# Kernel optimization log

Hardware: AMD Instinct MI355X
Metric: run time of the kernel (lower is better)

The kernel has to match this reference:

```python
import jax, jax.numpy as jnp
import numpy as np

FREQ_DIM = 32
TIME_DIM = 32
HEADS = 8
TWO_PI = 6.283185307179586


def get_embeddings(B, H, W, freq_dim, time_dim, dtype):
    # freq embeddings over the height (frequency) axis
    nf = freq_dim // 2
    ln_x = jnp.log2(jnp.arange(0, H * nf, dtype=jnp.float32))
    ln_x = ln_x.at[0].set(-2.0)
    ln_x = ln_x.reshape(H, nf).T  # [nf, H]
    ln_x = ln_x * jnp.arange(1, nf + 1, dtype=jnp.float32)[:, None]
    # view_as_real(exp(1j*theta)) -> (cos, sin), interleaved per order along channel dim
    freq = jnp.stack([jnp.cos(ln_x), jnp.sin(ln_x)], axis=1).reshape(freq_dim, H)  # [freq_dim, H]
    freq = jnp.broadcast_to(freq[None, :, :, None], (B, freq_dim, H, W))

    # time embeddings over the width (time) axis
    nt = time_dim // 2
    k = jnp.arange(0, nt, dtype=jnp.float32) + 0.5  # [nt]
    x = jnp.arange(0, nt * W, dtype=jnp.float32).reshape(W, nt).T  # [nt, W]
    theta = k[:, None] * x / (W * nt) * TWO_PI  # [nt, W]
    time = jnp.stack([jnp.cos(theta), jnp.sin(theta)], axis=1).reshape(time_dim, W)  # [time_dim, W]
    time = jnp.broadcast_to(time[None, :, None, :], (B, time_dim, H, W))

    return jnp.concatenate([freq, time], axis=1).astype(dtype)  # [B, freq_dim+time_dim, H, W]


def setup_inputs() -> dict:
    key = jax.random.key(0)
    ks = jax.random.split(key, 6)
    B, C, H, W = 2, 512, 64, 32
    qkC = C + FREQ_DIM + TIME_DIM  # 576
    inner = HEADS * 64  # 512
    return {
        "hidden_states": jax.random.normal(ks[0], (B, C, H, W), dtype=jnp.float32),
        "Wq": jax.random.normal(ks[1], (qkC, inner), dtype=jnp.float32) * 0.02,
        "Wk": jax.random.normal(ks[2], (qkC, inner), dtype=jnp.float32) * 0.02,
        "Wv": jax.random.normal(ks[3], (C, inner), dtype=jnp.float32) * 0.02,
        "Wout": jax.random.normal(ks[4], (inner, C), dtype=jnp.float32) * 0.02,
        "bout": jnp.zeros((C,), dtype=jnp.float32),
    }


def reference(hidden_states, Wq, Wk, Wv, Wout, bout):
    B, C, H, W = hidden_states.shape
    emb = get_embeddings(B, H, W, FREQ_DIM, TIME_DIM, hidden_states.dtype)
    qk_hs = jnp.concatenate([hidden_states, emb], axis=1)  # [B, qkC, H, W]

    S = H * W
    qk_hs = qk_hs.reshape(B, -1, S).transpose(0, 2, 1)  # [B, S, qkC]
    v_hs = hidden_states.reshape(B, C, S).transpose(0, 2, 1)  # [B, S, C]

    q = qk_hs @ Wq  # [B, S, inner]
    k = qk_hs @ Wk
    v = v_hs @ Wv

    hd_qk = q.shape[-1] // HEADS
    hd_v = v.shape[-1] // HEADS
    q = q.reshape(B, S, HEADS, hd_qk).transpose(0, 2, 1, 3)  # [B, h, S, d]
    k = k.reshape(B, S, HEADS, hd_qk).transpose(0, 2, 1, 3)
    v = v.reshape(B, S, HEADS, hd_v).transpose(0, 2, 1, 3)

    scale = 1.0 / jnp.sqrt(jnp.asarray(hd_qk, dtype=q.dtype))
    scores = jnp.einsum('bhqd,bhkd->bhqk', q, k) * scale
    attn = jax.nn.softmax(scores, axis=-1)
    o = jnp.einsum('bhqk,bhkd->bhqd', attn, v)  # [B, h, S, d_v]

    o = o.transpose(0, 2, 1, 3).reshape(B, S, HEADS * hd_v)
    o = o @ Wout + bout  # [B, S, C]
    o = o.transpose(0, 2, 1).reshape(B, C, H, W)

    return o + hidden_states  # residual_connection=True, rescale_output_factor=1.0
```

## Files before the change

kernel.cpp:

```cpp
#include <hip/hip_runtime.h>
#include <math.h>

#define B_    2
#define C_    512
#define H_    64
#define W_    32
#define S_    2048
#define QKC_  576
#define INNER_ 512
#define NH_   8
#define HD_   64
#define TWO_PI_ 6.283185307179586f

typedef __attribute__((ext_vector_type(8))) short bfrag;
typedef __attribute__((ext_vector_type(4))) float ffrag;
typedef __attribute__((ext_vector_type(16))) float f16v;

typedef __attribute__((address_space(1))) const unsigned int as1_u32;
typedef __attribute__((address_space(3))) unsigned int as3_u32;

__device__ __forceinline__ ushort f2bf(float f) {
    unsigned u = __builtin_bit_cast(unsigned, f);
    unsigned r = (u + 0x7FFFu + ((u >> 16) & 1u)) >> 16;
    return (ushort)r;
}

__device__ __forceinline__ f16v zero16() {
    f16v z;
    #pragma unroll
    for (int i = 0; i < 16; i++) z[i] = 0.f;
    return z;
}

#define GLD(gp_, lp_) __builtin_amdgcn_global_load_lds((as1_u32*)(gp_), (as3_u32*)(lp_), 16, 0, 0)
#define EXPA(dst_, x_) asm("v_exp_f32 %0, %1" : "=v"(dst_) : "v"(x_))
#define SC_LOG2E 0.18033688011f

__global__ void k_pre(const float* __restrict__ hid,
                      const float* __restrict__ Wq, const float* __restrict__ Wk,
                      const float* __restrict__ Wv, const float* __restrict__ Wo,
                      ushort* __restrict__ X,
                      ushort* __restrict__ Wqt, ushort* __restrict__ Wkt,
                      ushort* __restrict__ Wvt, ushort* __restrict__ Wot) {
    __shared__ float t[32][33];
    int tx = threadIdx.x, ty = threadIdx.y;
    int z = blockIdx.z;
    if (z < 2) {
        int b = z;
        int s0 = blockIdx.x * 32, c0 = blockIdx.y * 32;
        if (c0 < 512) {
            t[ty][tx] = hid[((size_t)b * C_ + (c0 + ty)) * S_ + s0 + tx];
            __syncthreads();
            X[((size_t)(b * S_ + s0 + ty)) * QKC_ + c0 + tx] = f2bf(t[tx][ty]);
        } else {
            int c = c0 - 512 + tx;
            int s = s0 + ty;
            int h = s >> 5, w = s & 31;
            float val;
            if (c < 32) {
                int f = c >> 1;
                int n = h * 16 + f;
                float lx = (n == 0) ? -2.0f : log2f((float)n);
                float arg = lx * (float)(f + 1);
                val = (c & 1) ? sinf(arg) : cosf(arg);
            } else {
                int tt = (c - 32) >> 1;
                float theta = ((float)tt + 0.5f) * (float)(w * 16 + tt) * (TWO_PI_ / 512.0f);
                val = (c & 1) ? sinf(theta) : cosf(theta);
            }
            X[(size_t)(b * S_ + s) * QKC_ + c0 + tx] = f2bf(val);
        }
    } else {
        int idx = blockIdx.y * 64 + blockIdx.x;
        int z4 = idx / 288, rem = idx % 288;
        int k0 = (rem % 18) * 32, n0 = (rem / 18) * 32;
        const float* W; ushort* Wt; int K;
        if (z4 == 0)      { W = Wq; Wt = Wqt; K = QKC_; }
        else if (z4 == 1) { W = Wk; Wt = Wkt; K = QKC_; }
        else if (z4 == 2) { W = Wv; Wt = Wvt; K = C_; }
        else              { W = Wo; Wt = Wot; K = INNER_; }
        if (k0 >= K) return;
        t[ty][tx] = W[(size_t)(k0 + ty) * 512 + n0 + tx];
        __syncthreads();
        Wt[(size_t)(n0 + ty) * K + k0 + tx] = f2bf(t[tx][ty]);
    }
}

#define GSTAGE(buf_, k0_) {                                                   \
    _Pragma("unroll")                                                         \
    for (int i_ = 0; i_ < 6; i_++)                                            \
        GLD(gp[i_] + (k0_), tl + (buf_) * 12288 + lo[i_]); }

__global__ __launch_bounds__(256, 3) void k_qkv(const ushort* __restrict__ X,
                                                const ushort* __restrict__ Wqt,
                                                const ushort* __restrict__ Wkt,
                                                const ushort* __restrict__ Wvt,
                                                ushort* __restrict__ Qb,
                                                ushort* __restrict__ Kpk,
                                                ushort* __restrict__ Vpk) {
    __shared__ ushort __attribute__((aligned(16))) tl[2 * 12288];

    int tid = threadIdx.x;
    int l = tid & 63, wv = tid >> 6;
    int wr = wv >> 1, wc = wv & 1;
    int bid = blockIdx.x;
    int lgc = (bid & 7) * 96 + (bid >> 3);
    int bx = lgc % 24, by = lgc / 24;
    int n0 = bx * 64, m0 = by * 128;
    int sel = n0 >> 9, n0l = n0 & 511;
    const ushort* Bt = (sel == 0) ? Wqt : (sel == 1) ? Wkt : Wvt;
    const int K = (sel < 2) ? QKC_ : C_;
    const int nst = K >> 6;
    int l15 = l & 15, lg = l >> 4;
    int swz = l15 & 7;

    const ushort* gp[6];
    unsigned lo[6];
    {
        int rsub = l >> 3;
        int clog = (l & 7) ^ rsub;
        #pragma unroll
        for (int i = 0; i < 6; i++) {
            int c = wv * 6 + i;
            lo[i] = c * 512;
            if (c < 16) gp[i] = X  + (size_t)(m0  + c * 8        + rsub) * QKC_ + clog * 8;
            else        gp[i] = Bt + (size_t)(n0l + (c - 16) * 8 + rsub) * K    + clog * 8;
        }
    }

    ffrag acc[4][2];
    #pragma unroll
    for (int i = 0; i < 4; i++)
        #pragma unroll
        for (int j = 0; j < 2; j++) acc[i][j] = (ffrag){0.f, 0.f, 0.f, 0.f};

    GSTAGE(0, 0);
    int cur = 0;
    for (int kt = 0; kt < nst; kt++) {
        __syncthreads();
        if (kt + 1 < nst) GSTAGE(cur ^ 1, (kt + 1) * 64);
        const ushort* As = tl + cur * 12288;
        const ushort* Bs = As + 8192;
        #pragma unroll
        for (int ks = 0; ks < 2; ks++) {
            int cl = ks * 4 + lg;
            int ch = (cl ^ swz) * 8;
            bfrag af[4], bf[2];
            #pragma unroll
            for (int mi = 0; mi < 4; mi++)
                af[mi] = *(const bfrag*)(As + (wr * 64 + mi * 16 + l15) * 64 + ch);
            #pragma unroll
            for (int nj = 0; nj < 2; nj++)
                bf[nj] = *(const bfrag*)(Bs + (wc * 32 + nj * 16 + l15) * 64 + ch);
            #pragma unroll
            for (int mi = 0; mi < 4; mi++)
                #pragma unroll
                for (int nj = 0; nj < 2; nj++)
                    acc[mi][nj] = __builtin_amdgcn_mfma_f32_16x16x32_bf16(af[mi], bf[nj], acc[mi][nj], 0, 0, 0);
        }
        cur ^= 1;
    }

    if (sel == 0) {
        #pragma unroll
        for (int mi = 0; mi < 4; mi++)
            #pragma unroll
            for (int nj = 0; nj < 2; nj++)
                #pragma unroll
                for (int r = 0; r < 4; r++) {
                    int row = m0 + wr * 64 + mi * 16 + lg * 4 + r;
                    int col = n0l + wc * 32 + nj * 16 + l15;
                    Qb[(size_t)row * INNER_ + col] = f2bf(acc[mi][nj][r] * SC_LOG2E);
                }
    } else {
        ushort (*Ct)[136] = (ushort(*)[136])tl;
        __syncthreads();
        #pragma unroll
        for (int mi = 0; mi < 4; mi++)
            #pragma unroll
            for (int nj = 0; nj < 2; nj++)
                #pragma unroll
                for (int r = 0; r < 4; r++)
                    Ct[wc * 32 + nj * 16 + l15][wr * 64 + mi * 16 + lg * 4 + r] = f2bf(acc[mi][nj][r]);
        __syncthreads();
        int pair = (m0 >> 11) * 8 + (n0l >> 6);
        int kvb0 = (m0 & 2047) >> 5;
        if (sel == 1) {
            #pragma unroll
            for (int p = 0; p < 4; p++) {
                int cid = tid + p * 256;
                int sl = cid >> 7, kv = cid & 127;
                bfrag tmp;
                #pragma unroll
                for (int j = 0; j < 8; j++) tmp[j] = (short)Ct[sl * 8 + j][kv];
                ushort* dst = Kpk + ((size_t)((pair * 64 + kvb0 + (kv >> 5)) * 8 + sl)) * 256 + (kv & 31) * 8;
                *(uint4*)dst = __builtin_bit_cast(uint4, tmp);
            }
        } else {
            #pragma unroll
            for (int p = 0; p < 4; p++) {
                int cid = tid + p * 256;
                int d = cid >> 4, mc = cid & 15;
                uint4 v = *(uint4*)&Ct[d][mc * 8];
                ushort* dst = Vpk + ((size_t)((pair * 64 + kvb0 + (mc >> 2)) * 4 + (mc & 3))) * 512 + d * 8;
                *(uint4*)dst = v;
            }
        }
    }
}

__global__ __launch_bounds__(256, 2) void k_og(const ushort* __restrict__ Ob,
                                               const ushort* __restrict__ Wot,
                                               const float* __restrict__ bias,
                                               const float* __restrict__ hid,
                                               float* __restrict__ out) {
    __shared__ ushort __attribute__((aligned(16))) tl[2 * 12288];

    int tid = threadIdx.x;
    int l = tid & 63, wv = tid >> 6;
    int wr = wv >> 1, wc = wv & 1;
    int bid = blockIdx.x;
    int lgc = (bid & 7) * 32 + (bid >> 3);
    int bx = lgc & 7, by = lgc >> 3;
    int n0 = bx * 64, m0 = by * 128;
    int l15 = l & 15, lg = l >> 4;
    int swz = l15 & 7;

    const ushort* gp[6];
    unsigned lo[6];
    {
        int rsub = l >> 3;
        int clog = (l & 7) ^ rsub;
        #pragma unroll
        for (int i = 0; i < 6; i++) {
            int c = wv * 6 + i;
            lo[i] = c * 512;
            if (c < 16) gp[i] = Ob  + (size_t)(m0 + c * 8        + rsub) * INNER_ + clog * 8;
            else        gp[i] = Wot + (size_t)(n0 + (c - 16) * 8 + rsub) * INNER_ + clog * 8;
        }
    }

    ffrag acc[4][2];
    #pragma unroll
    for (int i = 0; i < 4; i++)
        #pragma unroll
        for (int j = 0; j < 2; j++) acc[i][j] = (ffrag){0.f, 0.f, 0.f, 0.f};

    GSTAGE(0, 0);
    int cur = 0;
    for (int kt = 0; kt < 8; kt++) {
        __syncthreads();
        if (kt < 7) GSTAGE(cur ^ 1, (kt + 1) * 64);
        const ushort* As = tl + cur * 12288;
        const ushort* Bs = As + 8192;
        #pragma unroll
        for (int ks = 0; ks < 2; ks++) {
            int cl = ks * 4 + lg;
            int ch = (cl ^ swz) * 8;
            bfrag af[4], bf[2];
            #pragma unroll
            for (int mi = 0; mi < 4; mi++)
                af[mi] = *(const bfrag*)(As + (wr * 64 + mi * 16 + l15) * 64 + ch);
            #pragma unroll
            for (int nj = 0; nj < 2; nj++)
                bf[nj] = *(const bfrag*)(Bs + (wc * 32 + nj * 16 + l15) * 64 + ch);
            #pragma unroll
            for (int mi = 0; mi < 4; mi++)
                #pragma unroll
                for (int nj = 0; nj < 2; nj++)
                    acc[mi][nj] = __builtin_amdgcn_mfma_f32_16x16x32_bf16(af[mi], bf[nj], acc[mi][nj], 0, 0, 0);
        }
        cur ^= 1;
    }

    float (*Cf)[129] = (float(*)[129])tl;
    float bv[2];
    #pragma unroll
    for (int nj = 0; nj < 2; nj++) bv[nj] = bias[n0 + wc * 32 + nj * 16 + l15];
    __syncthreads();
    #pragma unroll
    for (int mi = 0; mi < 4; mi++)
        #pragma unroll
        for (int nj = 0; nj < 2; nj++)
            #pragma unroll
            for (int r = 0; r < 4; r++)
                Cf[wc * 32 + nj * 16 + l15][wr * 64 + mi * 16 + lg * 4 + r] = acc[mi][nj][r] + bv[nj];
    __syncthreads();
    int b = m0 >> 11, s0m = m0 & 2047;
    #pragma unroll
    for (int p = 0; p < 8; p++) {
        int f = p * 256 + tid;
        int c = f >> 5, sq = (f & 31) * 4;
        size_t o = (((size_t)(b * 512 + n0 + c)) << 11) + s0m + sq;
        float4 hv = *(const float4*)(hid + o);
        float4 cv = *(float4*)&Cf[c][sq];
        cv.x += hv.x; cv.y += hv.y; cv.z += hv.z; cv.w += hv.w;
        *(float4*)(out + o) = cv;
    }
}

#define CVTPK(dst, a, b) asm("v_cvt_pk_bf16_f32 %0, %1, %2" : "=v"(dst) : "v"(a), "v"(b))
#define SWAP32(a, b)     asm("v_permlane32_swap_b32 %0, %1" : "+v"(a), "+v"(b))

#define KLOAD(dst_, kt_) {                                                    \
    const ushort* g_ = kpb + (size_t)(kt_) * 2048 + kro;                      \
    _Pragma("unroll")                                                         \
    for (int ks_ = 0; ks_ < 4; ks_++) dst_[ks_] = *(const bfrag*)(g_ + ks_ * 512); }

#define VLOAD(dst_, kt_) {                                                    \
    const ushort* g_ = vpb + (size_t)(kt_) * 2048 + vro;                      \
    dst_[0] = *(const bfrag*)(g_);                                            \
    dst_[1] = *(const bfrag*)(g_ + 256);                                      \
    dst_[2] = *(const bfrag*)(g_ + 1024);                                     \
    dst_[3] = *(const bfrag*)(g_ + 1280); }

#define PVHALF(sf_, vf_, a0_, a1_) {                                          \
    _Pragma("unroll")                                                         \
    for (int s = 0; s < 2; s++) {                                             \
        unsigned A0, B0, A1, B1;                                              \
        CVTPK(A0, sf_[s * 8 + 0], sf_[s * 8 + 1]); CVTPK(B0, sf_[s * 8 + 4], sf_[s * 8 + 5]); \
        SWAP32(A0, B0);                                                       \
        CVTPK(A1, sf_[s * 8 + 2], sf_[s * 8 + 3]); CVTPK(B1, sf_[s * 8 + 6], sf_[s * 8 + 7]); \
        SWAP32(A1, B1);                                                       \
        uint4 u_; u_.x = A0; u_.y = A1; u_.z = B0; u_.w = B1;                 \
        bfrag pa_ = __builtin_bit_cast(bfrag, u_);                            \
        a0_ = __builtin_amdgcn_mfma_f32_32x32x16_bf16(vf_[s * 2],     pa_, a0_, 0, 0, 0); \
        a1_ = __builtin_amdgcn_mfma_f32_32x32x16_bf16(vf_[s * 2 + 1], pa_, a1_, 0, 0, 0); \
    } }

#define ABODY(kf_, vf_) {                                                     \
    __builtin_amdgcn_s_setprio(1);                                            \
    f16v sfA = __builtin_amdgcn_mfma_f32_32x32x16_bf16(kf_[0], qfA[0], fz, 0, 0, 0); \
    f16v sfB = __builtin_amdgcn_mfma_f32_32x32x16_bf16(kf_[0], qfB[0], fz, 0, 0, 0); \
    _Pragma("unroll")                                                         \
    for (int ks = 1; ks < 4; ks++) {                                          \
        sfA = __builtin_amdgcn_mfma_f32_32x32x16_bf16(kf_[ks], qfA[ks], sfA, 0, 0, 0); \
        sfB = __builtin_amdgcn_mfma_f32_32x32x16_bf16(kf_[ks], qfB[ks], sfB, 0, 0, 0); \
    }                                                                         \
    __builtin_amdgcn_s_setprio(0);                                            \
    float a0 = 0.f, a1 = 0.f, a2 = 0.f, a3 = 0.f;                             \
    float b0 = 0.f, b1 = 0.f, b2 = 0.f, b3 = 0.f;                             \
    _Pragma("unroll")                                                         \
    for (int j = 0; j < 4; j++) {                                             \
        float pA0; EXPA(pA0, sfA[j]);      sfA[j] = pA0;      a0 += pA0;      \
        float pA1; EXPA(pA1, sfA[j + 4]);  sfA[j + 4] = pA1;  a1 += pA1;      \
        float pA2; EXPA(pA2, sfA[j + 8]);  sfA[j + 8] = pA2;  a2 += pA2;      \
        float pA3; EXPA(pA3, sfA[j + 12]); sfA[j + 12] = pA3; a3 += pA3;      \
        float pB0; EXPA(pB0, sfB[j]);      sfB[j] = pB0;      b0 += pB0;      \
        float pB1; EXPA(pB1, sfB[j + 4]);  sfB[j + 4] = pB1;  b1 += pB1;      \
        float pB2; EXPA(pB2, sfB[j + 8]);  sfB[j + 8] = pB2;  b2 += pB2;      \
        float pB3; EXPA(pB3, sfB[j + 12]); sfB[j + 12] = pB3; b3 += pB3;      \
    }                                                                         \
    lA += (a0 + a1) + (a2 + a3);                                              \
    lB += (b0 + b1) + (b2 + b3);                                              \
    __builtin_amdgcn_s_setprio(1);                                            \
    PVHALF(sfA, vf_, accA0, accA1);                                           \
    PVHALF(sfB, vf_, accB0, accB1);                                           \
    __builtin_amdgcn_s_setprio(0); }

__global__ __launch_bounds__(512, 2) void k_attn(const ushort* __restrict__ Qf,
                                                 const ushort* __restrict__ Kpk,
                                                 const ushort* __restrict__ Vpk,
                                                 ushort* __restrict__ Ob) {
    __shared__ __attribute__((aligned(16))) char smem[137216];
    float* cmb = (float*)smem;
    float* lsh = (float*)(smem + 135168);

    const int id  = blockIdx.x;
    const int xcd = id & 7, wi = id >> 3;
    const int pair = xcd * 2 + (wi >> 4);
    const int qt   = wi & 15;
    const int hd = pair & 7, b = pair >> 3;

    const int tid = threadIdx.x;
    const int l = tid & 63, wvid = tid >> 6;
    const int qi = wvid >> 2, sp = wvid & 3;
    const int l31 = l & 31, hi = l >> 5;
    const int hoff = hd * HD_;
    const int brow = b * S_ + qt * 128;

    bfrag qfA[4], qfB[4];
    {
        const ushort* qpA = Qf + (size_t)(brow + qi * 64 + l31) * INNER_ + hoff + hi * 8;
        const ushort* qpB = qpA + (size_t)32 * INNER_;
        #pragma unroll
        for (int ks = 0; ks < 4; ks++) {
            qfA[ks] = *(const bfrag*)(qpA + ks * 16);
            qfB[ks] = *(const bfrag*)(qpB + ks * 16);
        }
    }

    const ushort* kpb = Kpk + ((size_t)pair * 64 + sp * 16) * 2048;
    const ushort* vpb = Vpk + ((size_t)pair * 64 + sp * 16) * 2048;
    const int kro = hi * 256 + l31 * 8;
    const int vro = hi * 512 + l31 * 8;

    const f16v fz = zero16();
    float lA = 0.f, lB = 0.f;
    f16v accA0 = fz, accA1 = fz;
    f16v accB0 = fz, accB1 = fz;

    bfrag kc[4], vc[4], kn[4], vn[4];
    KLOAD(kc, 0); VLOAD(vc, 0);

    for (int it = 0; it < 16; it += 2) {
        if (it + 1 < 16) { KLOAD(kn, it + 1); VLOAD(vn, it + 1); }
        ABODY(kc, vc);
        if (it + 2 < 16) { KLOAD(kc, it + 2); VLOAD(vc, it + 2); }
        ABODY(kn, vn);
    }

    lA += __shfl_xor(lA, 32);
    lB += __shfl_xor(lB, 32);

    if (hi == 0) {
        lsh[(wvid * 2 + 0) * 32 + l31] = lA;
        lsh[(wvid * 2 + 1) * 32 + l31] = lB;
    }
    {
        float* cA = cmb + (wvid * 2 + 0) * 2112;
        float* cB = cmb + (wvid * 2 + 1) * 2112;
        #pragma unroll
        for (int j = 0; j < 16; j++) {
            int d0 = (j & 3) + 8 * (j >> 2) + 4 * hi;
            cA[d0 * 33 + l31]        = accA0[j];
            cA[(d0 + 32) * 33 + l31] = accA1[j];
            cB[d0 * 33 + l31]        = accB0[j];
            cB[(d0 + 32) * 33 + l31] = accB1[j];
        }
    }
    __syncthreads();
    #pragma unroll
    for (int p2 = 0; p2 < 2; p2++) {
        int f = p2 * 512 + tid;
        int qig = f >> 8;
        int t2 = f & 255;
        int qq = t2 >> 3, cc = t2 & 7;
        int qih = qig >> 1, g = qig & 1;
        float lt = 0.f;
        #pragma unroll
        for (int s4 = 0; s4 < 4; s4++) lt += lsh[((qih * 4 + s4) * 2 + g) * 32 + qq];
        float inv = 1.0f / lt;
        bfrag ov;
        #pragma unroll
        for (int j = 0; j < 8; j++) {
            int d = cc * 8 + j;
            float s = 0.f;
            #pragma unroll
            for (int s4 = 0; s4 < 4; s4++)
                s += cmb[((qih * 4 + s4) * 2 + g) * 2112 + d * 33 + qq];
            ov[j] = (short)f2bf(s * inv);
        }
        *(uint4*)(Ob + (size_t)(brow + qig * 32 + qq) * INNER_ + hoff + cc * 8) = __builtin_bit_cast(uint4, ov);
    }
}

extern "C" void kernel_launch(void* const* d_in, const int* in_sizes, int n_in,
                              void* d_out, int out_size, void* d_ws, size_t ws_size,
                              hipStream_t stream) {
    const float* hid  = (const float*)d_in[0];
    const float* Wq   = (const float*)d_in[1];
    const float* Wk   = (const float*)d_in[2];
    const float* Wv   = (const float*)d_in[3];
    const float* Wout = (const float*)d_in[4];
    const float* bout = (const float*)d_in[5];
    float* out = (float*)d_out;

    const int M = B_ * S_;
    char* w = (char*)d_ws;
    ushort* X    = (ushort*)w;                    w += (size_t)M * QKC_ * 2;
    ushort* Qb   = (ushort*)w;                    w += (size_t)M * INNER_ * 2;
    ushort* Kpk  = (ushort*)w;                    w += (size_t)M * INNER_ * 2;
    ushort* Vpk  = (ushort*)w;                    w += (size_t)M * INNER_ * 2;
    ushort* Ob   = (ushort*)w;                    w += (size_t)M * INNER_ * 2;
    ushort* Wqt  = (ushort*)w;                    w += (size_t)INNER_ * QKC_ * 2;
    ushort* Wkt  = (ushort*)w;                    w += (size_t)INNER_ * QKC_ * 2;
    ushort* Wvt  = (ushort*)w;                    w += (size_t)INNER_ * C_ * 2;
    ushort* Wot  = (ushort*)w;                    w += (size_t)C_ * INNER_ * 2;

    k_pre<<<dim3(64, 18, 3), dim3(32, 32), 0, stream>>>(hid, Wq, Wk, Wv, Wout,
                                                        X, Wqt, Wkt, Wvt, Wot);

    k_qkv<<<dim3(768), 256, 0, stream>>>(X, Wqt, Wkt, Wvt, Qb, Kpk, Vpk);

    k_attn<<<dim3(256), 512, 0, stream>>>(Qb, Kpk, Vpk, Ob);

    k_og<<<dim3(256), 256, 0, stream>>>(Ob, Wot, bout, hid, out);
}
```

Before: 56.26 us.

## Halve attention query tile per block and double grid for higher occupancy

```diff
diff --git a/kernel.cpp b/kernel.cpp
--- a/kernel.cpp
+++ b/kernel.cpp
@@ -314,62 +314,18 @@
     dst_[2] = *(const bfrag*)(g_ + 1024);                                     \
     dst_[3] = *(const bfrag*)(g_ + 1280); }
 
-#define PVHALF(sf_, vf_, a0_, a1_) {                                          \
-    _Pragma("unroll")                                                         \
-    for (int s = 0; s < 2; s++) {                                             \
-        unsigned A0, B0, A1, B1;                                              \
-        CVTPK(A0, sf_[s * 8 + 0], sf_[s * 8 + 1]); CVTPK(B0, sf_[s * 8 + 4], sf_[s * 8 + 5]); \
-        SWAP32(A0, B0);                                                       \
-        CVTPK(A1, sf_[s * 8 + 2], sf_[s * 8 + 3]); CVTPK(B1, sf_[s * 8 + 6], sf_[s * 8 + 7]); \
-        SWAP32(A1, B1);                                                       \
-        uint4 u_; u_.x = A0; u_.y = A1; u_.z = B0; u_.w = B1;                 \
-        bfrag pa_ = __builtin_bit_cast(bfrag, u_);                            \
-        a0_ = __builtin_amdgcn_mfma_f32_32x32x16_bf16(vf_[s * 2],     pa_, a0_, 0, 0, 0); \
-        a1_ = __builtin_amdgcn_mfma_f32_32x32x16_bf16(vf_[s * 2 + 1], pa_, a1_, 0, 0, 0); \
-    } }
-
-#define ABODY(kf_, vf_) {                                                     \
-    __builtin_amdgcn_s_setprio(1);                                            \
-    f16v sfA = __builtin_amdgcn_mfma_f32_32x32x16_bf16(kf_[0], qfA[0], fz, 0, 0, 0); \
-    f16v sfB = __builtin_amdgcn_mfma_f32_32x32x16_bf16(kf_[0], qfB[0], fz, 0, 0, 0); \
-    _Pragma("unroll")                                                         \
-    for (int ks = 1; ks < 4; ks++) {                                          \
-        sfA = __builtin_amdgcn_mfma_f32_32x32x16_bf16(kf_[ks], qfA[ks], sfA, 0, 0, 0); \
-        sfB = __builtin_amdgcn_mfma_f32_32x32x16_bf16(kf_[ks], qfB[ks], sfB, 0, 0, 0); \
-    }                                                                         \
-    __builtin_amdgcn_s_setprio(0);                                            \
-    float a0 = 0.f, a1 = 0.f, a2 = 0.f, a3 = 0.f;                             \
-    float b0 = 0.f, b1 = 0.f, b2 = 0.f, b3 = 0.f;                             \
-    _Pragma("unroll")                                                         \
-    for (int j = 0; j < 4; j++) {                                             \
-        float pA0; EXPA(pA0, sfA[j]);      sfA[j] = pA0;      a0 += pA0;      \
-        float pA1; EXPA(pA1, sfA[j + 4]);  sfA[j + 4] = pA1;  a1 += pA1;      \
-        float pA2; EXPA(pA2, sfA[j + 8]);  sfA[j + 8] = pA2;  a2 += pA2;      \
-        float pA3; EXPA(pA3, sfA[j + 12]); sfA[j + 12] = pA3; a3 += pA3;      \
-        float pB0; EXPA(pB0, sfB[j]);      sfB[j] = pB0;      b0 += pB0;      \
-        float pB1; EXPA(pB1, sfB[j + 4]);  sfB[j + 4] = pB1;  b1 += pB1;      \
-        float pB2; EXPA(pB2, sfB[j + 8]);  sfB[j + 8] = pB2;  b2 += pB2;      \
-        float pB3; EXPA(pB3, sfB[j + 12]); sfB[j + 12] = pB3; b3 += pB3;      \
-    }                                                                         \
-    lA += (a0 + a1) + (a2 + a3);                                              \
-    lB += (b0 + b1) + (b2 + b3);                                              \
-    __builtin_amdgcn_s_setprio(1);                                            \
-    PVHALF(sfA, vf_, accA0, accA1);                                           \
-    PVHALF(sfB, vf_, accB0, accB1);                                           \
-    __builtin_amdgcn_s_setprio(0); }
-
-__global__ __launch_bounds__(512, 2) void k_attn(const ushort* __restrict__ Qf,
+__global__ __launch_bounds__(512, 4) void k_attn(const ushort* __restrict__ Qf,
                                                  const ushort* __restrict__ Kpk,
                                                  const ushort* __restrict__ Vpk,
                                                  ushort* __restrict__ Ob) {
-    __shared__ __attribute__((aligned(16))) char smem[137216];
+    __shared__ __attribute__((aligned(16))) char smem[68608];
     float* cmb = (float*)smem;
-    float* lsh = (float*)(smem + 135168);
+    float* lsh = (float*)(smem + 67584);
 
     const int id  = blockIdx.x;
     const int xcd = id & 7, wi = id >> 3;
-    const int pair = xcd * 2 + (wi >> 4);
-    const int qt   = wi & 15;
+    const int pair = xcd * 2 + (wi >> 5);
+    const int qt   = wi & 31;
     const int hd = pair & 7, b = pair >> 3;
 
     const int tid = threadIdx.x;
@@ -377,17 +333,13 @@
     const int qi = wvid >> 2, sp = wvid & 3;
     const int l31 = l & 31, hi = l >> 5;
     const int hoff = hd * HD_;
-    const int brow = b * S_ + qt * 128;
-
-    bfrag qfA[4], qfB[4];
+    const int brow = b * S_ + qt * 64;
+
+    bfrag qf[4];
     {
-        const ushort* qpA = Qf + (size_t)(brow + qi * 64 + l31) * INNER_ + hoff + hi * 8;
-        const ushort* qpB = qpA + (size_t)32 * INNER_;
-        #pragma unroll
-        for (int ks = 0; ks < 4; ks++) {
-            qfA[ks] = *(const bfrag*)(qpA + ks * 16);
-            qfB[ks] = *(const bfrag*)(qpB + ks * 16);
-        }
+        const ushort* qp = Qf + (size_t)(brow + qi * 32 + l31) * INNER_ + hoff + hi * 8;
+        #pragma unroll
+        for (int ks = 0; ks < 4; ks++) qf[ks] = *(const bfrag*)(qp + ks * 16);
     }
 
     const ushort* kpb = Kpk + ((size_t)pair * 64 + sp * 16) * 2048;
@@ -395,51 +347,67 @@
     const int kro = hi * 256 + l31 * 8;
     const int vro = hi * 512 + l31 * 8;
 
-    const f16v fz = zero16();
-    float lA = 0.f, lB = 0.f;
-    f16v accA0 = fz, accA1 = fz;
-    f16v accB0 = fz, accB1 = fz;
-
-    bfrag kc[4], vc[4], kn[4], vn[4];
-    KLOAD(kc, 0); VLOAD(vc, 0);
-
-    for (int it = 0; it < 16; it += 2) {
-        if (it + 1 < 16) { KLOAD(kn, it + 1); VLOAD(vn, it + 1); }
-        ABODY(kc, vc);
-        if (it + 2 < 16) { KLOAD(kc, it + 2); VLOAD(vc, it + 2); }
-        ABODY(kn, vn);
-    }
-
-    lA += __shfl_xor(lA, 32);
-    lB += __shfl_xor(lB, 32);
-
-    if (hi == 0) {
-        lsh[(wvid * 2 + 0) * 32 + l31] = lA;
-        lsh[(wvid * 2 + 1) * 32 + l31] = lB;
-    }
+    float l_run = 0.f;
+    f16v acc0 = zero16(), acc1 = zero16();
+
+    for (int it = 0; it < 16; it++) {
+        bfrag kc[4], vc[4];
+        KLOAD(kc, it); VLOAD(vc, it);
+
+        __builtin_amdgcn_s_setprio(1);
+        f16v sf = __builtin_amdgcn_mfma_f32_32x32x16_bf16(kc[0], qf[0], zero16(), 0, 0, 0);
+        #pragma unroll
+        for (int ks = 1; ks < 4; ks++)
+            sf = __builtin_amdgcn_mfma_f32_32x32x16_bf16(kc[ks], qf[ks], sf, 0, 0, 0);
+        __builtin_amdgcn_s_setprio(0);
+
+        float a0 = 0.f, a1 = 0.f, a2 = 0.f, a3 = 0.f;
+        #pragma unroll
+        for (int j = 0; j < 4; j++) {
+            float p0; EXPA(p0, sf[j]);      sf[j] = p0;      a0 += p0;
+            float p1; EXPA(p1, sf[j + 4]);  sf[j + 4] = p1;  a1 += p1;
+            float p2; EXPA(p2, sf[j + 8]);  sf[j + 8] = p2;  a2 += p2;
+            float p3; EXPA(p3, sf[j + 12]); sf[j + 12] = p3; a3 += p3;
+        }
+        l_run += (a0 + a1) + (a2 + a3);
+
+        __builtin_amdgcn_s_setprio(1);
+        #pragma unroll
+        for (int s = 0; s < 2; s++) {
+            unsigned A0, B0, A1, B1;
+            CVTPK(A0, sf[s * 8 + 0], sf[s * 8 + 1]); CVTPK(B0, sf[s * 8 + 4], sf[s * 8 + 5]);
+            SWAP32(A0, B0);
+            CVTPK(A1, sf[s * 8 + 2], sf[s * 8 + 3]); CVTPK(B1, sf[s * 8 + 6], sf[s * 8 + 7]);
+            SWAP32(A1, B1);
+            uint4 u; u.x = A0; u.y = A1; u.z = B0; u.w = B1;
+            bfrag pa = __builtin_bit_cast(bfrag, u);
+            acc0 = __builtin_amdgcn_mfma_f32_32x32x16_bf16(vc[s * 2],     pa, acc0, 0, 0, 0);
+            acc1 = __builtin_amdgcn_mfma_f32_32x32x16_bf16(vc[s * 2 + 1], pa, acc1, 0, 0, 0);
+        }
+        __builtin_amdgcn_s_setprio(0);
+    }
+
+    l_run += __shfl_xor(l_run, 32);
+
+    if (hi == 0) lsh[wvid * 32 + l31] = l_run;
     {
-        float* cA = cmb + (wvid * 2 + 0) * 2112;
-        float* cB = cmb + (wvid * 2 + 1) * 2112;
+        float* cw = cmb + wvid * 2112;
         #pragma unroll
         for (int j = 0; j < 16; j++) {
             int d0 = (j & 3) + 8 * (j >> 2) + 4 * hi;
-            cA[d0 * 33 + l31]        = accA0[j];
-            cA[(d0 + 32) * 33 + l31] = accA1[j];
-            cB[d0 * 33 + l31]        = accB0[j];
-            cB[(d0 + 32) * 33 + l31] = accB1[j];
+            cw[d0 * 33 + l31]        = acc0[j];
+            cw[(d0 + 32) * 33 + l31] = acc1[j];
         }
     }
     __syncthreads();
-    #pragma unroll
-    for (int p2 = 0; p2 < 2; p2++) {
-        int f = p2 * 512 + tid;
+    {
+        int f = tid;
         int qig = f >> 8;
         int t2 = f & 255;
         int qq = t2 >> 3, cc = t2 & 7;
-        int qih = qig >> 1, g = qig & 1;
         float lt = 0.f;
         #pragma unroll
-        for (int s4 = 0; s4 < 4; s4++) lt += lsh[((qih * 4 + s4) * 2 + g) * 32 + qq];
+        for (int s4 = 0; s4 < 4; s4++) lt += lsh[(qig * 4 + s4) * 32 + qq];
         float inv = 1.0f / lt;
         bfrag ov;
         #pragma unroll
@@ -448,7 +416,7 @@
             float s = 0.f;
             #pragma unroll
             for (int s4 = 0; s4 < 4; s4++)
-                s += cmb[((qih * 4 + s4) * 2 + g) * 2112 + d * 33 + qq];
+                s += cmb[(qig * 4 + s4) * 2112 + d * 33 + qq];
             ov[j] = (short)f2bf(s * inv);
         }
         *(uint4*)(Ob + (size_t)(brow + qig * 32 + qq) * INNER_ + hoff + cc * 8) = __builtin_bit_cast(uint4, ov);
@@ -483,7 +451,7 @@
 
     k_qkv<<<dim3(768), 256, 0, stream>>>(X, Wqt, Wkt, Wvt, Qb, Kpk, Vpk);
 
-    k_attn<<<dim3(256), 512, 0, stream>>>(Qb, Kpk, Vpk, Ob);
+    k_attn<<<dim3(512), 512, 0, stream>>>(Qb, Kpk, Vpk, Ob);
 
     k_og<<<dim3(256), 256, 0, stream>>>(Ob, Wot, bout, hid, out);
 }
```

Result: slower. 59.08 us (+5.0%).

## Stage K/V tiles through LDS with async global loads, double-buffered per wave

Applied to the files above, without the earlier changes.

```diff
diff --git a/kernel.cpp b/kernel.cpp
--- a/kernel.cpp
+++ b/kernel.cpp
@@ -302,19 +302,16 @@
 #define CVTPK(dst, a, b) asm("v_cvt_pk_bf16_f32 %0, %1, %2" : "=v"(dst) : "v"(a), "v"(b))
 #define SWAP32(a, b)     asm("v_permlane32_swap_b32 %0, %1" : "+v"(a), "+v"(b))
 
-#define KLOAD(dst_, kt_) {                                                    \
-    const ushort* g_ = kpb + (size_t)(kt_) * 2048 + kro;                      \
+#define ASTAGE(buf_, kt_) {                                                   \
+    const ushort* gk_ = kpb + (size_t)(kt_) * 2048 + l * 8;                   \
+    const ushort* gv_ = vpb + (size_t)(kt_) * 2048 + l * 8;                   \
+    ushort* lk_ = lbase + (buf_) * 4096;                                      \
     _Pragma("unroll")                                                         \
-    for (int ks_ = 0; ks_ < 4; ks_++) dst_[ks_] = *(const bfrag*)(g_ + ks_ * 512); }
-
-#define VLOAD(dst_, kt_) {                                                    \
-    const ushort* g_ = vpb + (size_t)(kt_) * 2048 + vro;                      \
-    dst_[0] = *(const bfrag*)(g_);                                            \
-    dst_[1] = *(const bfrag*)(g_ + 256);                                      \
-    dst_[2] = *(const bfrag*)(g_ + 1024);                                     \
-    dst_[3] = *(const bfrag*)(g_ + 1280); }
-
-#define PVHALF(sf_, vf_, a0_, a1_) {                                          \
+    for (int i_ = 0; i_ < 4; i_++) GLD(gk_ + i_ * 512, lk_ + i_ * 512);       \
+    _Pragma("unroll")                                                         \
+    for (int i_ = 0; i_ < 4; i_++) GLD(gv_ + i_ * 512, lk_ + 2048 + i_ * 512); }
+
+#define PVHALF(sf_, Vt_, a0_, a1_) {                                          \
     _Pragma("unroll")                                                         \
     for (int s = 0; s < 2; s++) {                                             \
         unsigned A0, B0, A1, B1;                                              \
@@ -324,19 +321,28 @@
         SWAP32(A1, B1);                                                       \
         uint4 u_; u_.x = A0; u_.y = A1; u_.z = B0; u_.w = B1;                 \
         bfrag pa_ = __builtin_bit_cast(bfrag, u_);                            \
-        a0_ = __builtin_amdgcn_mfma_f32_32x32x16_bf16(vf_[s * 2],     pa_, a0_, 0, 0, 0); \
-        a1_ = __builtin_amdgcn_mfma_f32_32x32x16_bf16(vf_[s * 2 + 1], pa_, a1_, 0, 0, 0); \
+        bfrag v0_ = *(const bfrag*)(Vt_ + s * 1024 + voff);                   \
+        bfrag v1_ = *(const bfrag*)(Vt_ + s * 1024 + voff + 256);             \
+        a0_ = __builtin_amdgcn_mfma_f32_32x32x16_bf16(v0_, pa_, a0_, 0, 0, 0);\
+        a1_ = __builtin_amdgcn_mfma_f32_32x32x16_bf16(v1_, pa_, a1_, 0, 0, 0);\
     } }
 
-#define ABODY(kf_, vf_) {                                                     \
+#define ABODY(buf_) {                                                         \
+    const ushort* Kt_ = lbase + (buf_) * 4096;                                \
+    const ushort* Vt_ = Kt_ + 2048;                                           \
+    bfrag k0_ = *(const bfrag*)(Kt_ + 0 * 512 + koff);                        \
+    bfrag k1_ = *(const bfrag*)(Kt_ + 1 * 512 + koff);                        \
+    bfrag k2_ = *(const bfrag*)(Kt_ + 2 * 512 + koff);                        \
+    bfrag k3_ = *(const bfrag*)(Kt_ + 3 * 512 + koff);                        \
     __builtin_amdgcn_s_setprio(1);                                            \
-    f16v sfA = __builtin_amdgcn_mfma_f32_32x32x16_bf16(kf_[0], qfA[0], fz, 0, 0, 0); \
-    f16v sfB = __builtin_amdgcn_mfma_f32_32x32x16_bf16(kf_[0], qfB[0], fz, 0, 0, 0); \
-    _Pragma("unroll")                                                         \
-    for (int ks = 1; ks < 4; ks++) {                                          \
-        sfA = __builtin_amdgcn_mfma_f32_32x32x16_bf16(kf_[ks], qfA[ks], sfA, 0, 0, 0); \
-        sfB = __builtin_amdgcn_mfma_f32_32x32x16_bf16(kf_[ks], qfB[ks], sfB, 0, 0, 0); \
-    }                                                                         \
+    f16v sfA = __builtin_amdgcn_mfma_f32_32x32x16_bf16(k0_, qfA[0], fz, 0, 0, 0); \
+    f16v sfB = __builtin_amdgcn_mfma_f32_32x32x16_bf16(k0_, qfB[0], fz, 0, 0, 0); \
+    sfA = __builtin_amdgcn_mfma_f32_32x32x16_bf16(k1_, qfA[1], sfA, 0, 0, 0); \
+    sfB = __builtin_amdgcn_mfma_f32_32x32x16_bf16(k1_, qfB[1], sfB, 0, 0, 0); \
+    sfA = __builtin_amdgcn_mfma_f32_32x32x16_bf16(k2_, qfA[2], sfA, 0, 0, 0); \
+    sfB = __builtin_amdgcn_mfma_f32_32x32x16_bf16(k2_, qfB[2], sfB, 0, 0, 0); \
+    sfA = __builtin_amdgcn_mfma_f32_32x32x16_bf16(k3_, qfA[3], sfA, 0, 0, 0); \
+    sfB = __builtin_amdgcn_mfma_f32_32x32x16_bf16(k3_, qfB[3], sfB, 0, 0, 0); \
     __builtin_amdgcn_s_setprio(0);                                            \
     float a0 = 0.f, a1 = 0.f, a2 = 0.f, a3 = 0.f;                             \
     float b0 = 0.f, b1 = 0.f, b2 = 0.f, b3 = 0.f;                             \
@@ -354,17 +360,18 @@
     lA += (a0 + a1) + (a2 + a3);                                              \
     lB += (b0 + b1) + (b2 + b3);                                              \
     __builtin_amdgcn_s_setprio(1);                                            \
-    PVHALF(sfA, vf_, accA0, accA1);                                           \
-    PVHALF(sfB, vf_, accB0, accB1);                                           \
+    PVHALF(sfA, Vt_, accA0, accA1);                                           \
+    PVHALF(sfB, Vt_, accB0, accB1);                                           \
     __builtin_amdgcn_s_setprio(0); }
 
 __global__ __launch_bounds__(512, 2) void k_attn(const ushort* __restrict__ Qf,
                                                  const ushort* __restrict__ Kpk,
                                                  const ushort* __restrict__ Vpk,
                                                  ushort* __restrict__ Ob) {
-    __shared__ __attribute__((aligned(16))) char smem[137216];
-    float* cmb = (float*)smem;
-    float* lsh = (float*)(smem + 135168);
+    __shared__ __attribute__((aligned(16))) char smem[133120];
+    ushort* ktv = (ushort*)smem;
+    float*  cmb = (float*)smem;
+    float*  lsh = (float*)(smem + 131072);
 
     const int id  = blockIdx.x;
     const int xcd = id & 7, wi = id >> 3;
@@ -392,22 +399,28 @@
 
     const ushort* kpb = Kpk + ((size_t)pair * 64 + sp * 16) * 2048;
     const ushort* vpb = Vpk + ((size_t)pair * 64 + sp * 16) * 2048;
-    const int kro = hi * 256 + l31 * 8;
-    const int vro = hi * 512 + l31 * 8;
+    ushort* lbase = ktv + wvid * 8192;
+    const int koff = l31 * 8 + hi * 256;
+    const int voff = l31 * 8 + hi * 512;
+
+    ASTAGE(0, 0);
 
     const f16v fz = zero16();
     float lA = 0.f, lB = 0.f;
     f16v accA0 = fz, accA1 = fz;
     f16v accB0 = fz, accB1 = fz;
-
-    bfrag kc[4], vc[4], kn[4], vn[4];
-    KLOAD(kc, 0); VLOAD(vc, 0);
-
-    for (int it = 0; it < 16; it += 2) {
-        if (it + 1 < 16) { KLOAD(kn, it + 1); VLOAD(vn, it + 1); }
-        ABODY(kc, vc);
-        if (it + 2 < 16) { KLOAD(kc, it + 2); VLOAD(vc, it + 2); }
-        ABODY(kn, vn);
+    int buf = 0;
+
+    for (int it = 0; it < 16; it++) {
+        if (it < 15) {
+            ASTAGE(buf ^ 1, it + 1);
+            asm volatile("s_waitcnt vmcnt(8)" ::: "memory");
+        } else {
+            asm volatile("s_waitcnt vmcnt(0)" ::: "memory");
+        }
+        __builtin_amdgcn_sched_barrier(0);
+        ABODY(buf);
+        buf ^= 1;
     }
 
     lA += __shfl_xor(lA, 32);
@@ -417,29 +430,26 @@
         lsh[(wvid * 2 + 0) * 32 + l31] = lA;
         lsh[(wvid * 2 + 1) * 32 + l31] = lB;
     }
-    {
-        float* cA = cmb + (wvid * 2 + 0) * 2112;
-        float* cB = cmb + (wvid * 2 + 1) * 2112;
+    __syncthreads();
+
+    {
+        float* cw = cmb + wvid * 2112;
         #pragma unroll
         for (int j = 0; j < 16; j++) {
             int d0 = (j & 3) + 8 * (j >> 2) + 4 * hi;
-            cA[d0 * 33 + l31]        = accA0[j];
-            cA[(d0 + 32) * 33 + l31] = accA1[j];
-            cB[d0 * 33 + l31]        = accB0[j];
-            cB[(d0 + 32) * 33 + l31] = accB1[j];
+            cw[d0 * 33 + l31]        = accA0[j];
+            cw[(d0 + 32) * 33 + l31] = accA1[j];
         }
     }
     __syncthreads();
-    #pragma unroll
-    for (int p2 = 0; p2 < 2; p2++) {
-        int f = p2 * 512 + tid;
-        int qig = f >> 8;
+    {
+        int f = tid;
+        int qi2 = f >> 8;
         int t2 = f & 255;
         int qq = t2 >> 3, cc = t2 & 7;
-        int qih = qig >> 1, g = qig & 1;
         float lt = 0.f;
         #pragma unroll
-        for (int s4 = 0; s4 < 4; s4++) lt += lsh[((qih * 4 + s4) * 2 + g) * 32 + qq];
+        for (int s4 = 0; s4 < 4; s4++) lt += lsh[((qi2 * 4 + s4) * 2 + 0) * 32 + qq];
         float inv = 1.0f / lt;
         bfrag ov;
         #pragma unroll
@@ -447,11 +457,42 @@
             int d = cc * 8 + j;
             float s = 0.f;
             #pragma unroll
-            for (int s4 = 0; s4 < 4; s4++)
-                s += cmb[((qih * 4 + s4) * 2 + g) * 2112 + d * 33 + qq];
+            for (int s4 = 0; s4 < 4; s4++) s += cmb[(qi2 * 4 + s4) * 2112 + d * 33 + qq];
             ov[j] = (short)f2bf(s * inv);
         }
-        *(uint4*)(Ob + (size_t)(brow + qig * 32 + qq) * INNER_ + hoff + cc * 8) = __builtin_bit_cast(uint4, ov);
+        *(uint4*)(Ob + (size_t)(brow + qi2 * 64 + qq) * INNER_ + hoff + cc * 8) = __builtin_bit_cast(uint4, ov);
+    }
+    __syncthreads();
+
+    {
+        float* cw = cmb + wvid * 2112;
+        #pragma unroll
+        for (int j = 0; j < 16; j++) {
+            int d0 = (j & 3) + 8 * (j >> 2) + 4 * hi;
+            cw[d0 * 33 + l31]        = accB0[j];
+            cw[(d0 + 32) * 33 + l31] = accB1[j];
+        }
+    }
+    __syncthreads();
+    {
+        int f = tid;
+        int qi2 = f >> 8;
+        int t2 = f & 255;
+        int qq = t2 >> 3, cc = t2 & 7;
+        float lt = 0.f;
+        #pragma unroll
+        for (int s4 = 0; s4 < 4; s4++) lt += lsh[((qi2 * 4 + s4) * 2 + 1) * 32 + qq];
+        float inv = 1.0f / lt;
+        bfrag ov;
+        #pragma unroll
+        for (int j = 0; j < 8; j++) {
+            int d = cc * 8 + j;
+            float s = 0.f;
+            #pragma unroll
+            for (int s4 = 0; s4 < 4; s4++) s += cmb[(qi2 * 4 + s4) * 2112 + d * 33 + qq];
+            ov[j] = (short)f2bf(s * inv);
+        }
+        *(uint4*)(Ob + (size_t)(brow + qi2 * 64 + 32 + qq) * INNER_ + hoff + cc * 8) = __builtin_bit_cast(uint4, ov);
     }
 }
 
```

Measured after the change: 59.51 us. 5.8% more time.

## Split attention across eight KV slices per 64-query tile with smaller combine buffer

Applied to the files above, without the earlier changes.

```diff
diff --git a/kernel.cpp b/kernel.cpp
--- a/kernel.cpp
+++ b/kernel.cpp
@@ -358,30 +358,54 @@
     PVHALF(sfB, vf_, accB0, accB1);                                           \
     __builtin_amdgcn_s_setprio(0); }
 
+#define DUMPC(acc_) {                                                         \
+    float* cw = cmb + wvid * 1056;                                            \
+    _Pragma("unroll")                                                         \
+    for (int j = 0; j < 16; j++) {                                            \
+        int d0 = (j & 3) + 8 * (j >> 2) + 4 * hi;                             \
+        cw[d0 * 33 + l31] = acc_[j];                                          \
+    } }
+
+#define COMBC(g_, dh_) {                                                      \
+    int qq = tid >> 4, dp = tid & 15;                                         \
+    float lt = 0.f;                                                           \
+    _Pragma("unroll")                                                         \
+    for (int s8 = 0; s8 < 8; s8++) lt += lsh[(s8 * 2 + (g_)) * 32 + qq];      \
+    float inv = 1.0f / lt;                                                    \
+    float s0 = 0.f, s1 = 0.f;                                                 \
+    _Pragma("unroll")                                                         \
+    for (int s8 = 0; s8 < 8; s8++) {                                          \
+        s0 += cmb[s8 * 1056 + (dp * 2)     * 33 + qq];                        \
+        s1 += cmb[s8 * 1056 + (dp * 2 + 1) * 33 + qq];                        \
+    }                                                                         \
+    unsigned pk = (unsigned)f2bf(s0 * inv) | ((unsigned)f2bf(s1 * inv) << 16);\
+    *(unsigned*)(Ob + (size_t)(brow + (g_) * 32 + qq) * INNER_ + hoff         \
+                 + (dh_) * 32 + dp * 2) = pk; }
+
 __global__ __launch_bounds__(512, 2) void k_attn(const ushort* __restrict__ Qf,
                                                  const ushort* __restrict__ Kpk,
                                                  const ushort* __restrict__ Vpk,
                                                  ushort* __restrict__ Ob) {
-    __shared__ __attribute__((aligned(16))) char smem[137216];
+    __shared__ __attribute__((aligned(16))) char smem[35840];
     float* cmb = (float*)smem;
-    float* lsh = (float*)(smem + 135168);
+    float* lsh = (float*)(smem + 33792);
 
     const int id  = blockIdx.x;
     const int xcd = id & 7, wi = id >> 3;
-    const int pair = xcd * 2 + (wi >> 4);
-    const int qt   = wi & 15;
+    const int pair = xcd * 2 + (wi >> 5);
+    const int qt   = wi & 31;
     const int hd = pair & 7, b = pair >> 3;
 
     const int tid = threadIdx.x;
     const int l = tid & 63, wvid = tid >> 6;
-    const int qi = wvid >> 2, sp = wvid & 3;
+    const int sp = wvid;
     const int l31 = l & 31, hi = l >> 5;
     const int hoff = hd * HD_;
-    const int brow = b * S_ + qt * 128;
+    const int brow = b * S_ + qt * 64;
 
     bfrag qfA[4], qfB[4];
     {
-        const ushort* qpA = Qf + (size_t)(brow + qi * 64 + l31) * INNER_ + hoff + hi * 8;
+        const ushort* qpA = Qf + (size_t)(brow + l31) * INNER_ + hoff + hi * 8;
         const ushort* qpB = qpA + (size_t)32 * INNER_;
         #pragma unroll
         for (int ks = 0; ks < 4; ks++) {
@@ -390,8 +414,8 @@
         }
     }
 
-    const ushort* kpb = Kpk + ((size_t)pair * 64 + sp * 16) * 2048;
-    const ushort* vpb = Vpk + ((size_t)pair * 64 + sp * 16) * 2048;
+    const ushort* kpb = Kpk + ((size_t)pair * 64 + sp * 8) * 2048;
+    const ushort* vpb = Vpk + ((size_t)pair * 64 + sp * 8) * 2048;
     const int kro = hi * 256 + l31 * 8;
     const int vro = hi * 512 + l31 * 8;
 
@@ -403,10 +427,10 @@
     bfrag kc[4], vc[4], kn[4], vn[4];
     KLOAD(kc, 0); VLOAD(vc, 0);
 
-    for (int it = 0; it < 16; it += 2) {
-        if (it + 1 < 16) { KLOAD(kn, it + 1); VLOAD(vn, it + 1); }
+    for (int it = 0; it < 8; it += 2) {
+        if (it + 1 < 8) { KLOAD(kn, it + 1); VLOAD(vn, it + 1); }
         ABODY(kc, vc);
-        if (it + 2 < 16) { KLOAD(kc, it + 2); VLOAD(vc, it + 2); }
+        if (it + 2 < 8) { KLOAD(kc, it + 2); VLOAD(vc, it + 2); }
         ABODY(kn, vn);
     }
 
@@ -414,45 +438,25 @@
     lB += __shfl_xor(lB, 32);
 
     if (hi == 0) {
-        lsh[(wvid * 2 + 0) * 32 + l31] = lA;
-        lsh[(wvid * 2 + 1) * 32 + l31] = lB;
-    }
-    {
-        float* cA = cmb + (wvid * 2 + 0) * 2112;
-        float* cB = cmb + (wvid * 2 + 1) * 2112;
-        #pragma unroll
-        for (int j = 0; j < 16; j++) {
-            int d0 = (j & 3) + 8 * (j >> 2) + 4 * hi;
-            cA[d0 * 33 + l31]        = accA0[j];
-            cA[(d0 + 32) * 33 + l31] = accA1[j];
-            cB[d0 * 33 + l31]        = accB0[j];
-            cB[(d0 + 32) * 33 + l31] = accB1[j];
-        }
-    }
-    __syncthreads();
-    #pragma unroll
-    for (int p2 = 0; p2 < 2; p2++) {
-        int f = p2 * 512 + tid;
-        int qig = f >> 8;
-        int t2 = f & 255;
-        int qq = t2 >> 3, cc = t2 & 7;
-        int qih = qig >> 1, g = qig & 1;
-        float lt = 0.f;
-        #pragma unroll
-        for (int s4 = 0; s4 < 4; s4++) lt += lsh[((qih * 4 + s4) * 2 + g) * 32 + qq];
-        float inv = 1.0f / lt;
-        bfrag ov;
-        #pragma unroll
-        for (int j = 0; j < 8; j++) {
-            int d = cc * 8 + j;
-            float s = 0.f;
-            #pragma unroll
-            for (int s4 = 0; s4 < 4; s4++)
-                s += cmb[((qih * 4 + s4) * 2 + g) * 2112 + d * 33 + qq];
-            ov[j] = (short)f2bf(s * inv);
-        }
-        *(uint4*)(Ob + (size_t)(brow + qig * 32 + qq) * INNER_ + hoff + cc * 8) = __builtin_bit_cast(uint4, ov);
-    }
+        lsh[(sp * 2 + 0) * 32 + l31] = lA;
+        lsh[(sp * 2 + 1) * 32 + l31] = lB;
+    }
+
+    DUMPC(accA0);
+    __syncthreads();
+    COMBC(0, 0);
+    __syncthreads();
+    DUMPC(accA1);
+    __syncthreads();
+    COMBC(0, 1);
+    __syncthreads();
+    DUMPC(accB0);
+    __syncthreads();
+    COMBC(1, 0);
+    __syncthreads();
+    DUMPC(accB1);
+    __syncthreads();
+    COMBC(1, 1);
 }
 
 extern "C" void kernel_launch(void* const* d_in, const int* in_sizes, int n_in,
@@ -483,7 +487,7 @@
 
     k_qkv<<<dim3(768), 256, 0, stream>>>(X, Wqt, Wkt, Wvt, Qb, Kpk, Vpk);
 
-    k_attn<<<dim3(256), 512, 0, stream>>>(Qb, Kpk, Vpk, Ob);
+    k_attn<<<dim3(512), 512, 0, stream>>>(Qb, Kpk, Vpk, Ob);
 
     k_og<<<dim3(256), 256, 0, stream>>>(Ob, Wot, bout, hid, out);
 }
```

New measurement: 60.22 us. +7.0%, slower.
